# Optimization experiments

Hardware: AMD Instinct MI355X
Metric: run time of the kernel (lower is better)

The kernel has to match this reference:

```python
import jax, jax.numpy as jnp
import numpy as np

L, Q = 256, 21
LAMBDA_H = 1e-06
LAMBDA_J = 0.0001
M = 8192


def setup_inputs() -> dict:
    key = jax.random.key(0)
    k1, k2, k3, k4 = jax.random.split(key, 4)
    seqs = jax.random.randint(k1, (M, L), 0, Q, dtype=jnp.int64 if jax.config.jax_enable_x64 else jnp.int32)
    weights = jax.random.uniform(k2, (M,), dtype=jnp.float32)
    h = jax.random.normal(k3, (L, Q), dtype=jnp.float32) * 0.1
    J = jax.random.normal(k4, (L, L, Q, Q), dtype=jnp.float32) * 0.02
    return {"seqs": seqs, "weights": weights, "h": h, "J": J}


def reference(seqs, weights, h, J):
    # strictly-lower-triangular mask over (i, j): j < i
    tril = jnp.tril(jnp.ones((L, L), dtype=bool), k=-1)
    Jm = J * tril[:, :, None, None]                       # (L, L, q, q)

    # one-hot history; H[b, j, k] = 1 iff seqs[b, j] == k
    H = jax.nn.one_hot(seqs, Q, dtype=h.dtype)            # (M, L, q)

    # contrib[b, i, a] = sum_{j<i, k} J[i, j, a, k] * H[b, j, k]
    # == one big (M, L*q) x (L*q, L*q) causal-masked matmul
    contrib = jnp.einsum('ijak,bjk->bia', Jm, H)          # (M, L, q)

    logits = h[None, :, :] + contrib                      # (M, L, q)
    logp = jax.nn.log_softmax(logits, axis=-1)            # (M, L, q)

    # gather label log-probs
    ll = jnp.take_along_axis(logp, seqs[..., None], axis=-1)[..., 0]  # (M, L)

    M_eff = jnp.maximum(weights.sum(), 1e-12)
    w_norm = weights / M_eff
    nll = -(w_norm[:, None] * ll).sum()

    reg_h = 0.5 * LAMBDA_H * jnp.sum(h ** 2)
    reg_J = 0.5 * LAMBDA_J * jnp.sum(Jm ** 2)
    loss = nll + reg_h + reg_J
    return (loss, nll, reg_h + reg_J)
```

## Files before the change

kernel.cpp:

```cpp
#include <hip/hip_runtime.h>
#include <cstdint>
#include <cstddef>

#define L_   256
#define Q_   21
#define M_   8192
#define QQ   441
#define JCH  32
#define SCALE    32.0f
#define INVSCALE 0.03125f
#define NPAIR ((L_ * (L_ - 1)) / 2)
#define PPB   16
#define PREPB (NPAIR / PPB)


typedef float v2f __attribute__((ext_vector_type(2)));

__device__ __forceinline__ float block_reduce_sum(float v) {
    __shared__ float s[256];
    int t = threadIdx.x;
    __syncthreads();
    s[t] = v;
    __syncthreads();
#pragma unroll
    for (int o = 128; o > 0; o >>= 1) {
        if (t < o) s[t] += s[t + o];
        __syncthreads();
    }
    return s[0];
}

__device__ __forceinline__ int tri_invert(int n) {
    int i = (int)((1.0f + sqrtf(8.0f * (float)n + 1.0f)) * 0.5f);
    while (i * (i - 1) / 2 > n) --i;
    while (i * (i - 1) / 2 + i <= n) ++i;
    return i;
}

__global__ __launch_bounds__(256) void k_prep(const float* __restrict__ J,
                                              unsigned* __restrict__ Jt,
                                              float* __restrict__ acc) {
    __shared__ float sB[PPB * QQ];
    const int t = threadIdx.x;
    const int n0 = blockIdx.x * PPB;

    float v2acc = 0.f;
#pragma unroll 1
    for (int p = 0; p < PPB; ++p) {
        const int n = n0 + p;
        const int i = tri_invert(n);
        const int j = n - i * (i - 1) / 2;
        const float* blk = J + ((size_t)i * L_ + j) * QQ;
        float* dst = sB + p * QQ;
        for (int x = t; x < QQ; x += 256) {
            float v = blk[x];
            dst[x] = v;
            v2acc += v * v;
        }
    }
    __syncthreads();

    {
        const int p = t >> 4;
        const int n = n0 + p;
        const int i = tri_invert(n);
        const int j = n - i * (i - 1) / 2;
        const size_t ij = (size_t)i * L_ + j;
        const float* s = sB + p * QQ;
#pragma unroll
        for (int u = 0; u < 8; ++u) {
            const int d = (t & 15) + (u << 4);
            const int kr = d / 6;
            const int dw = d - 6 * kr;
            const int a0 = dw * 4;
            unsigned outw = 0;
            if (kr < Q_) {
                float x0 = (a0 + 0 < Q_) ? s[(a0 + 0) * Q_ + kr] : 0.f;
                float x1 = (a0 + 1 < Q_) ? s[(a0 + 1) * Q_ + kr] : 0.f;
                float x2 = (a0 + 2 < Q_) ? s[(a0 + 2) * Q_ + kr] : 0.f;
                float x3 = (a0 + 3 < Q_) ? s[(a0 + 3) * Q_ + kr] : 0.f;
                outw = (unsigned)__builtin_amdgcn_cvt_pk_fp8_f32(x0 * SCALE, x1 * SCALE, 0, false);
                outw = (unsigned)__builtin_amdgcn_cvt_pk_fp8_f32(x2 * SCALE, x3 * SCALE, (int)outw, true);
            }
            Jt[ij * 128 + d] = outw;
        }
    }

    float r = block_reduce_sum(v2acc);
    if (t == 0) atomicAdd(&acc[4 + (blockIdx.x & 255)], r);
}

__global__ __launch_bounds__(256) void k_prep2(const int* __restrict__ seqs,
                                               const float* __restrict__ w,
                                               const float* __restrict__ h,
                                               unsigned* __restrict__ seqsP,
                                               float* __restrict__ acc) {
    const int bid = blockIdx.x;
    const int t = threadIdx.x;
    if (bid < 32) {
        const int b = bid * 256 + t;
        const int4* row = reinterpret_cast<const int4*>(seqs + (size_t)b * L_);
#pragma unroll 4
        for (int jq = 0; jq < L_ / 4; ++jq) {
            int4 v = row[jq];
            unsigned p = (unsigned)(v.x & 255) | ((unsigned)(v.y & 255) << 8) |
                         ((unsigned)(v.z & 255) << 16) | ((unsigned)(v.w & 255) << 24);
            seqsP[jq * M_ + b] = p;
        }
    } else {
        float v = 0.f;
        for (int x = t; x < M_; x += 256) v += w[x];
        float r = block_reduce_sum(v);
        if (t == 0) acc[0] = r;
        float v2 = 0.f;
        for (int x = t; x < L_ * Q_; x += 256) { float y = h[x]; v2 += y * y; }
        float r2 = block_reduce_sum(v2);
        if (t == 0) acc[2] = r2;
    }
}

#define BODY(jj)                                                                   \
    {                                                                              \
        const unsigned kk = (idxw[(jj) >> 2] >> (((jj) & 3) * 8)) & 255u;          \
        const uint2* r = reinterpret_cast<const uint2*>(sJ) + ((jj) * 64 + kk * 3);\
        uint2 d0 = r[0], d1 = r[1], d2 = r[2];                                     \
        acc2[0]  += __builtin_amdgcn_cvt_pk_f32_fp8(d0.x, false);                  \
        acc2[1]  += __builtin_amdgcn_cvt_pk_f32_fp8(d0.x, true);                   \
        acc2[2]  += __builtin_amdgcn_cvt_pk_f32_fp8(d0.y, false);                  \
        acc2[3]  += __builtin_amdgcn_cvt_pk_f32_fp8(d0.y, true);                   \
        acc2[4]  += __builtin_amdgcn_cvt_pk_f32_fp8(d1.x, false);                  \
        acc2[5]  += __builtin_amdgcn_cvt_pk_f32_fp8(d1.x, true);                   \
        acc2[6]  += __builtin_amdgcn_cvt_pk_f32_fp8(d1.y, false);                  \
        acc2[7]  += __builtin_amdgcn_cvt_pk_f32_fp8(d1.y, true);                   \
        acc2[8]  += __builtin_amdgcn_cvt_pk_f32_fp8(d2.x, false);                  \
        acc2[9]  += __builtin_amdgcn_cvt_pk_f32_fp8(d2.x, true);                   \
        acc2[10] += __builtin_amdgcn_cvt_pk_f32_fp8(d2.y, false);                  \
    }

__global__ __launch_bounds__(256, 8) void k_main(const unsigned* __restrict__ Jt,
                                                 const float* __restrict__ h,
                                                 const unsigned* __restrict__ seqsP,
                                                 const float* __restrict__ weights,
                                                 float* __restrict__ acc) {
    __shared__ unsigned sJ[JCH * 128];

    const int bid = blockIdx.x;
    const int i = (L_ - 1) - (bid >> 5);
    const int b = ((bid & 31) << 8) + threadIdx.x;

    v2f acc2[11];
    const float* hp = h + i * Q_;
#pragma unroll
    for (int m = 0; m < 10; ++m) { acc2[m].x = hp[2*m] * SCALE; acc2[m].y = hp[2*m+1] * SCALE; }
    acc2[10].x = hp[20] * SCALE; acc2[10].y = 0.f;

    const unsigned* Jrow = Jt + (size_t)i * (256 * 128);

    const int nStages = i >> 5;
    const int rem     = i & 31;

    for (int s = 0; s < nStages; ++s) {
        const int j0 = s << 5;
        {
            const uint4* src = reinterpret_cast<const uint4*>(Jrow + j0 * 128);
            uint4* dst = reinterpret_cast<uint4*>(sJ);
#pragma unroll
            for (int n = 0; n < (JCH * 32) / 256; ++n) {
                dst[n * 256 + threadIdx.x] = src[n * 256 + threadIdx.x];
            }
        }
        __syncthreads();

        unsigned idxw[JCH / 4];
#pragma unroll
        for (int q = 0; q < JCH / 4; ++q) {
            idxw[q] = seqsP[((j0 >> 2) + q) * M_ + b];
        }

#pragma unroll
        for (int jj = 0; jj < JCH; ++jj) BODY(jj);

        __syncthreads();
    }

    if (rem) {
        const int j0 = nStages << 5;
        {
            const uint4* src = reinterpret_cast<const uint4*>(Jrow + j0 * 128);
            uint4* dst = reinterpret_cast<uint4*>(sJ);
#pragma unroll
            for (int n = 0; n < (JCH * 32) / 256; ++n) {
                dst[n * 256 + threadIdx.x] = src[n * 256 + threadIdx.x];
            }
        }
        __syncthreads();

        unsigned idxw[JCH / 4];
#pragma unroll
        for (int q = 0; q < JCH / 4; ++q) {
            idxw[q] = seqsP[((j0 >> 2) + q) * M_ + b];
        }

#pragma unroll
        for (int jj = 0; jj < JCH; ++jj) {
            if (jj >= rem) break;
            BODY(jj);
        }
    }

    float l[21];
#pragma unroll
    for (int m = 0; m < 10; ++m) { l[2*m] = acc2[m].x * INVSCALE; l[2*m+1] = acc2[m].y * INVSCALE; }
    l[20] = acc2[10].x * INVSCALE;

    unsigned lw = seqsP[(i >> 2) * M_ + b];
    int lbl = (int)((lw >> ((i & 3) * 8)) & 255u);

    float m = l[0];
#pragma unroll
    for (int a = 1; a < 21; ++a) m = fmaxf(m, l[a]);
    float s = 0.f;
    float lv = l[0];
#pragma unroll
    for (int a = 0; a < 21; ++a) {
        s += __expf(l[a] - m);
        if (a > 0) lv = (a == lbl) ? l[a] : lv;
    }
    float ll = (lv - m) - __logf(s);
    float contrib = weights[b] * ll;

    float r = block_reduce_sum(contrib);
    if (threadIdx.x == 0) atomicAdd(&acc[260 + (bid & 127)], r);
}

__global__ void k_final(const float* __restrict__ acc, float* __restrict__ out) {
    int t = threadIdx.x;
    float j2p = acc[4 + t];
    float j2 = block_reduce_sum(j2p);
    float llp = (t < 128) ? acc[260 + t] : 0.f;
    float lls = block_reduce_sum(llp);
    if (t == 0) {
        float wsum = fmaxf(acc[0], 1e-12f);
        float nll = -lls / wsum;
        float reg = 0.5e-6f * acc[2] + 0.5e-4f * j2;
        out[0] = nll + reg;
        out[1] = nll;
        out[2] = reg;
    }
}

extern "C" void kernel_launch(void* const* d_in, const int* in_sizes, int n_in,
                              void* d_out, int out_size, void* d_ws, size_t ws_size,
                              hipStream_t stream) {
    const int*   seqs    = (const int*)d_in[0];
    const float* weights = (const float*)d_in[1];
    const float* h       = (const float*)d_in[2];
    const float* J       = (const float*)d_in[3];
    float* out = (float*)d_out;

    char* ws = (char*)d_ws;
    float*    acc   = (float*)ws;
    unsigned* seqsP = (unsigned*)(ws + 2048);
    unsigned* Jt    = (unsigned*)(ws + 2048 + (size_t)(L_ / 4) * M_ * sizeof(unsigned));

    hipMemsetAsync(d_ws, 0, 2048, stream);

    k_prep<<<PREPB, 256, 0, stream>>>(J, Jt, acc);
    k_prep2<<<33, 256, 0, stream>>>(seqs, weights, h, seqsP, acc);
    k_main<<<L_ * (M_ / 256), 256, 0, stream>>>(Jt, h, seqsP, weights, acc);
    k_final<<<1, 256, 0, stream>>>(acc, out);
}
```

Before: 429.0 us.

## Switch packed J storage from fp8 to fp16 with packed half accumulation

Stores the transposed J blocks as fp16 pairs instead of fp8 quads, doubling the per-(i,j) footprint to 256 words, and accumulates logits in packed half2 registers with plain adds instead of fp8-to-fp32 conversions. The shared-memory chunk is halved to 16 j-columns so LDS use stays the same. The aim is to remove the conversion instructions from the inner loop. In exchange it doubles J bandwidth and staging traffic, doubles the number of stage barriers, and accumulating up to 255 terms in fp16 risks precision loss.

```diff
diff --git a/kernel.cpp b/kernel.cpp
--- a/kernel.cpp
+++ b/kernel.cpp
@@ -6,7 +6,7 @@
 #define Q_   21
 #define M_   8192
 #define QQ   441
-#define JCH  32
+#define JCH  16
 #define SCALE    32.0f
 #define INVSCALE 0.03125f
 #define NPAIR ((L_ * (L_ - 1)) / 2)
@@ -14,7 +14,7 @@
 #define PREPB (NPAIR / PPB)
 
 
-typedef float v2f __attribute__((ext_vector_type(2)));
+typedef _Float16 h2 __attribute__((ext_vector_type(2)));
 
 __device__ __forceinline__ float block_reduce_sum(float v) {
     __shared__ float s[256];
@@ -68,21 +68,21 @@
         const size_t ij = (size_t)i * L_ + j;
         const float* s = sB + p * QQ;
 #pragma unroll
-        for (int u = 0; u < 8; ++u) {
+        for (int u = 0; u < 16; ++u) {
             const int d = (t & 15) + (u << 4);
-            const int kr = d / 6;
-            const int dw = d - 6 * kr;
-            const int a0 = dw * 4;
+            const int kr = d / 12;
+            const int dw = d - 12 * kr;
+            const int a0 = dw * 2;
             unsigned outw = 0;
             if (kr < Q_) {
                 float x0 = (a0 + 0 < Q_) ? s[(a0 + 0) * Q_ + kr] : 0.f;
                 float x1 = (a0 + 1 < Q_) ? s[(a0 + 1) * Q_ + kr] : 0.f;
-                float x2 = (a0 + 2 < Q_) ? s[(a0 + 2) * Q_ + kr] : 0.f;
-                float x3 = (a0 + 3 < Q_) ? s[(a0 + 3) * Q_ + kr] : 0.f;
-                outw = (unsigned)__builtin_amdgcn_cvt_pk_fp8_f32(x0 * SCALE, x1 * SCALE, 0, false);
-                outw = (unsigned)__builtin_amdgcn_cvt_pk_fp8_f32(x2 * SCALE, x3 * SCALE, (int)outw, true);
+                union { _Float16 hh[2]; unsigned u; } uu;
+                uu.hh[0] = (_Float16)(x0 * SCALE);
+                uu.hh[1] = (_Float16)(x1 * SCALE);
+                outw = uu.u;
             }
-            Jt[ij * 128 + d] = outw;
+            Jt[ij * 256 + d] = outw;
         }
     }
 
@@ -119,22 +119,18 @@
     }
 }
 
-#define BODY(jj)                                                                   \
-    {                                                                              \
-        const unsigned kk = (idxw[(jj) >> 2] >> (((jj) & 3) * 8)) & 255u;          \
-        const uint2* r = reinterpret_cast<const uint2*>(sJ) + ((jj) * 64 + kk * 3);\
-        uint2 d0 = r[0], d1 = r[1], d2 = r[2];                                     \
-        acc2[0]  += __builtin_amdgcn_cvt_pk_f32_fp8(d0.x, false);                  \
-        acc2[1]  += __builtin_amdgcn_cvt_pk_f32_fp8(d0.x, true);                   \
-        acc2[2]  += __builtin_amdgcn_cvt_pk_f32_fp8(d0.y, false);                  \
-        acc2[3]  += __builtin_amdgcn_cvt_pk_f32_fp8(d0.y, true);                   \
-        acc2[4]  += __builtin_amdgcn_cvt_pk_f32_fp8(d1.x, false);                  \
-        acc2[5]  += __builtin_amdgcn_cvt_pk_f32_fp8(d1.x, true);                   \
-        acc2[6]  += __builtin_amdgcn_cvt_pk_f32_fp8(d1.y, false);                  \
-        acc2[7]  += __builtin_amdgcn_cvt_pk_f32_fp8(d1.y, true);                   \
-        acc2[8]  += __builtin_amdgcn_cvt_pk_f32_fp8(d2.x, false);                  \
-        acc2[9]  += __builtin_amdgcn_cvt_pk_f32_fp8(d2.x, true);                   \
-        acc2[10] += __builtin_amdgcn_cvt_pk_f32_fp8(d2.y, false);                  \
+#define BODY(jj)                                                                    \
+    {                                                                               \
+        const unsigned kk = (idxw[(jj) >> 2] >> (((jj) & 3) * 8)) & 255u;           \
+        const uint4* rp = reinterpret_cast<const uint4*>(sJ) + ((jj) * 64 + kk * 3);\
+        union { uint4 u; h2 h[4]; } ra, rb, rc;                                     \
+        ra.u = rp[0]; rb.u = rp[1]; rc.u = rp[2];                                   \
+        acch[0]  += ra.h[0]; acch[1]  += ra.h[1];                                   \
+        acch[2]  += ra.h[2]; acch[3]  += ra.h[3];                                   \
+        acch[4]  += rb.h[0]; acch[5]  += rb.h[1];                                   \
+        acch[6]  += rb.h[2]; acch[7]  += rb.h[3];                                   \
+        acch[8]  += rc.h[0]; acch[9]  += rc.h[1];                                   \
+        acch[10] += rc.h[2]; acch[11] += rc.h[3];                                   \
     }
 
 __global__ __launch_bounds__(256, 8) void k_main(const unsigned* __restrict__ Jt,
@@ -142,30 +138,34 @@
                                                  const unsigned* __restrict__ seqsP,
                                                  const float* __restrict__ weights,
                                                  float* __restrict__ acc) {
-    __shared__ unsigned sJ[JCH * 128];
+    __shared__ unsigned sJ[JCH * 256];
 
     const int bid = blockIdx.x;
     const int i = (L_ - 1) - (bid >> 5);
     const int b = ((bid & 31) << 8) + threadIdx.x;
 
-    v2f acc2[11];
+    h2 acch[12];
     const float* hp = h + i * Q_;
 #pragma unroll
-    for (int m = 0; m < 10; ++m) { acc2[m].x = hp[2*m] * SCALE; acc2[m].y = hp[2*m+1] * SCALE; }
-    acc2[10].x = hp[20] * SCALE; acc2[10].y = 0.f;
-
-    const unsigned* Jrow = Jt + (size_t)i * (256 * 128);
-
-    const int nStages = i >> 5;
-    const int rem     = i & 31;
+    for (int m = 0; m < 10; ++m) {
+        acch[m].x = (_Float16)(hp[2 * m] * SCALE);
+        acch[m].y = (_Float16)(hp[2 * m + 1] * SCALE);
+    }
+    acch[10].x = (_Float16)(hp[20] * SCALE); acch[10].y = (_Float16)0.f;
+    acch[11].x = (_Float16)0.f;              acch[11].y = (_Float16)0.f;
+
+    const unsigned* Jrow = Jt + (size_t)i * (256 * 256);
+
+    const int nStages = i >> 4;
+    const int rem     = i & 15;
 
     for (int s = 0; s < nStages; ++s) {
-        const int j0 = s << 5;
+        const int j0 = s << 4;
         {
-            const uint4* src = reinterpret_cast<const uint4*>(Jrow + j0 * 128);
+            const uint4* src = reinterpret_cast<const uint4*>(Jrow + j0 * 256);
             uint4* dst = reinterpret_cast<uint4*>(sJ);
 #pragma unroll
-            for (int n = 0; n < (JCH * 32) / 256; ++n) {
+            for (int n = 0; n < 4; ++n) {
                 dst[n * 256 + threadIdx.x] = src[n * 256 + threadIdx.x];
             }
         }
@@ -184,12 +184,12 @@
     }
 
     if (rem) {
-        const int j0 = nStages << 5;
+        const int j0 = nStages << 4;
         {
-            const uint4* src = reinterpret_cast<const uint4*>(Jrow + j0 * 128);
+            const uint4* src = reinterpret_cast<const uint4*>(Jrow + j0 * 256);
             uint4* dst = reinterpret_cast<uint4*>(sJ);
 #pragma unroll
-            for (int n = 0; n < (JCH * 32) / 256; ++n) {
+            for (int n = 0; n < 4; ++n) {
                 dst[n * 256 + threadIdx.x] = src[n * 256 + threadIdx.x];
             }
         }
@@ -210,8 +210,11 @@
 
     float l[21];
 #pragma unroll
-    for (int m = 0; m < 10; ++m) { l[2*m] = acc2[m].x * INVSCALE; l[2*m+1] = acc2[m].y * INVSCALE; }
-    l[20] = acc2[10].x * INVSCALE;
+    for (int m = 0; m < 10; ++m) {
+        l[2 * m]     = (float)acch[m].x * INVSCALE;
+        l[2 * m + 1] = (float)acch[m].y * INVSCALE;
+    }
+    l[20] = (float)acch[10].x * INVSCALE;
 
     unsigned lw = seqsP[(i >> 2) * M_ + b];
     int lbl = (int)((lw >> ((i & 3) * 8)) & 255u);
```

After: 416.8 us. 1.03x faster.
